# Optimization experiments

Hardware: AMD Instinct MI355X
Metric: run time of the kernel (lower is better)

## Reference

```python
import jax, jax.numpy as jnp
import numpy as np

B, R, S, C, H, MLP = 4, 32, 4, 128, 4, 512  # batch, resolution, box_size, dim, heads, mlp_dim
N = S ** 3            # tokens per window = 64
NW = (R // S) ** 3    # windows per batch element = 512
SHIFT = S // 2


def _layernorm(x, g, b):
    m = jnp.mean(x, axis=-1, keepdims=True)
    v = jnp.var(x, axis=-1, keepdims=True)
    return (x - m) * jax.lax.rsqrt(v + 1e-5) * g + b


def _box_partition(x):
    # x: (b, R, R, R, C) -> (b*NW, N, C)
    b = x.shape[0]
    x = x.reshape(b, R // S, S, R // S, S, R // S, S, C)
    x = x.transpose(0, 1, 3, 5, 2, 4, 6, 7)
    return x.reshape(-1, N, C)


def _box_reverse(w, b):
    # w: (b*NW, N, C) -> (b, R, R, R, C)
    x = w.reshape(b, R // S, R // S, R // S, S, S, S, C)
    x = x.transpose(0, 1, 4, 2, 5, 3, 6, 7)
    return x.reshape(b, R, R, R, C)


def setup_inputs():
    key = jax.random.key(0)
    ks = jax.random.split(key, 8)
    f = lambda k, sh: jax.random.normal(k, sh, dtype=jnp.float32) * 0.02
    x = jax.random.normal(ks[0], (B, R ** 3, C), dtype=jnp.float32)
    qkv_w = f(ks[1], (3 * C, C))
    rpb_table = f(ks[2], ((3 * S - 1) ** 3, H))
    proj_w = f(ks[3], (C, C))
    proj_b = jnp.zeros((C,), jnp.float32)
    norm1_g = jnp.ones((C,), jnp.float32)
    norm1_b = jnp.zeros((C,), jnp.float32)
    norm2_g = jnp.ones((C,), jnp.float32)
    norm2_b = jnp.zeros((C,), jnp.float32)
    mlp_w1 = f(ks[4], (MLP, C))
    mlp_b1 = jnp.zeros((MLP,), jnp.float32)
    mlp_w2 = f(ks[5], (C, MLP))
    mlp_b2 = jnp.zeros((C,), jnp.float32)
    # relative position index (N, N), int constant
    coords = np.stack(np.meshgrid(*([np.arange(S)] * 3), indexing='ij')).reshape(3, -1)
    rel = coords[:, :, None] - coords[:, None, :]
    rel = rel.transpose(1, 2, 0) + (S - 1)
    rel[..., 0] *= (2 * S - 1) ** 2
    rel[..., 1] *= (2 * S - 1)
    rel_index = jnp.asarray(rel.sum(-1), jnp.int32)
    # shifted-window additive attention mask (NW, N, N)
    img = np.zeros((1, R, R, R, 1), np.float32)
    sl = (slice(0, -S), slice(-S, -SHIFT), slice(-SHIFT, None))
    cnt = 0
    for a in sl:
        for b2 in sl:
            for c in sl:
                img[:, a, b2, c, :] = cnt
                cnt += 1
    m = img.reshape(1, R // S, S, R // S, S, R // S, S, 1)
    m = m.transpose(0, 1, 3, 5, 2, 4, 6, 7).reshape(-1, N)
    am = m[:, None, :] - m[:, :, None]
    attn_mask = jnp.asarray(np.where(am != 0, -100.0, 0.0).astype(np.float32))
    return dict(x=x, qkv_w=qkv_w, rpb_table=rpb_table, proj_w=proj_w, proj_b=proj_b,
                norm1_g=norm1_g, norm1_b=norm1_b, norm2_g=norm2_g, norm2_b=norm2_b,
                mlp_w1=mlp_w1, mlp_b1=mlp_b1, mlp_w2=mlp_w2, mlp_b2=mlp_b2,
                attn_mask=attn_mask, rel_index=rel_index)


def reference(x, qkv_w, rpb_table, proj_w, proj_b, norm1_g, norm1_b,
              norm2_g, norm2_b, mlp_w1, mlp_b1, mlp_w2, mlp_b2,
              attn_mask, rel_index):
    scale = (C // H) ** -0.5
    shortcut = x
    xn = _layernorm(x, norm1_g, norm1_b).reshape(B, R, R, R, C)
    xs = jnp.roll(xn, (-SHIFT,) * 3, axis=(1, 2, 3))
    w = _box_partition(xs)  # (B*NW, N, C)
    qkv = (w @ qkv_w.T).reshape(-1, N, 3, H, C // H).transpose(2, 0, 3, 1, 4)
    q, k, v = qkv[0] * scale, qkv[1], qkv[2]  # (B*NW, H, N, hd)
    attn = jnp.einsum('whnd,whmd->whnm', q, k)
    bias = rpb_table[rel_index].transpose(2, 0, 1)  # (H, N, N)
    attn = attn + bias[None]
    attn = attn.reshape(B, NW, H, N, N) + attn_mask[None, :, None]
    attn = jax.nn.softmax(attn.reshape(-1, H, N, N), axis=-1)
    out = jnp.einsum('whnm,whmd->whnd', attn, v).transpose(0, 2, 1, 3).reshape(-1, N, C)
    out = out @ proj_w.T + proj_b
    xm = _box_reverse(out, B)
    xm = jnp.roll(xm, (SHIFT,) * 3, axis=(1, 2, 3)).reshape(B, -1, C)
    x1 = shortcut + 0.5 * xm
    h = _layernorm(x1, norm2_g, norm2_b)
    h = jax.nn.gelu(h @ mlp_w1.T + mlp_b1, approximate=False) @ mlp_w2.T + mlp_b2
    return x1 + 0.5 * h
```

## Files before the change

kernel.cpp:

```cpp
#include <hip/hip_runtime.h>
#include <hip/hip_bf16.h>

typedef unsigned short u16;
typedef unsigned int u32;
typedef short bf16x8 __attribute__((ext_vector_type(8)));
typedef float f32x4 __attribute__((ext_vector_type(4)));

__device__ __forceinline__ u16 f2bf(float f) {
  union { float f; u32 i; } v; v.f = f;
  u32 x = v.i;
  x += 0x7fff + ((x >> 16) & 1);
  return (u16)(x >> 16);
}
__device__ __forceinline__ u32 pack2(float a, float b) {
  return (u32)f2bf(a) | ((u32)f2bf(b) << 16);
}
__device__ __forceinline__ u32 cvtpk2(float a, float b) {
  __hip_bfloat162 t = __float22bfloat162_rn(float2{a, b});
  union { __hip_bfloat162 h; u32 u; } v; v.h = t; return v.u;
}
__device__ __forceinline__ float fastrcp(float x) {
  float r;
  asm("v_rcp_f32 %0, %1" : "=v"(r) : "v"(x));
  return r;
}

#define L2E 1.4426950408889634f


__global__ void prep_kernel(const float* __restrict__ rpb, const int* __restrict__ rel,
                            const float* __restrict__ qkv_w, const float* __restrict__ proj_w,
                            const float* __restrict__ w1, const float* __restrict__ w2,
                            float* __restrict__ bias_t, u16* __restrict__ qkv_f,
                            u16* __restrict__ proj_f, u16* __restrict__ w1f,
                            u16* __restrict__ w2f) {
  const int bid = blockIdx.x;
  if (bid < 64) {
    const int idx = bid * 256 + threadIdx.x;
    const int h = idx >> 12, rm = idx & 4095;
    const int r = rm >> 6, c = rm & 63;
    bias_t[h * 4096 + c * 64 + r] = rpb[rel[rm] * 4 + h] * L2E;
    return;
  }
  const int i4 = (bid - 64) * 256 + threadIdx.x;
  const int e = i4 * 4;
  const float scale = 0.17677669529663687f * L2E;
  float4 v; u16* dst;
  if (e < 49152) {
    v = *(const float4*)(qkv_w + e);
    if (e < 16384) { v.x *= scale; v.y *= scale; v.z *= scale; v.w *= scale; }
    const int row = e >> 7, col = e & 127;
    const int tile = (row >> 4) * 4 + (col >> 5);
    const int lane = ((col >> 3) & 3) * 16 + (row & 15);
    dst = qkv_f + tile * 512 + lane * 8 + (col & 7);
  } else if (e < 65536) {
    const int le = e - 49152;
    v = *(const float4*)(proj_w + le);
    const int row = le >> 7, col = le & 127;
    const int tile = (row >> 4) * 4 + (col >> 5);
    const int lane = ((col >> 3) & 3) * 16 + (row & 15);
    dst = proj_f + tile * 512 + lane * 8 + (col & 7);
  } else if (e < 131072) {
    const int le = e - 65536;
    v = *(const float4*)(w1 + le);
    const int row = le >> 7, col = le & 127;
    const int tile = (row >> 4) * 4 + (col >> 5);
    const int lane = ((col >> 3) & 3) * 16 + (row & 15);
    dst = w1f + tile * 512 + lane * 8 + (col & 7);
  } else {
    const int le = e - 131072;
    v = *(const float4*)(w2 + le);
    const int row = le >> 9, col = le & 511;
    const int tile = (row >> 4) * 16 + (col >> 5);
    const int lane = ((col >> 3) & 3) * 16 + (row & 15);
    dst = w2f + tile * 512 + lane * 8 + (col & 7);
  }
  *(uint2*)dst = make_uint2(pack2(v.x, v.y), pack2(v.z, v.w));
}

__global__ __launch_bounds__(512, 4) void fused_kernel(
    const float* __restrict__ x, const u16* __restrict__ qkv_f,
    const u16* __restrict__ proj_f, const float* __restrict__ proj_b,
    const float* __restrict__ n1g, const float* __restrict__ n1b,
    const float* __restrict__ amask, const float* __restrict__ bias_t,
    const u16* __restrict__ w1f, const float* __restrict__ b1,
    const u16* __restrict__ w2f, const float* __restrict__ b2,
    const float* __restrict__ n2g, const float* __restrict__ n2b,
    float* __restrict__ out)
{
  __shared__ __align__(16) unsigned char lds[70656];
  __shared__ int srcIdx[64];
  u16* xw = (u16*)(lds);
  u16* qb = (u16*)(lds + 17408);
  u16* kb = (u16*)(lds + 34816);
  u16* vt = (u16*)(lds + 52224);
  unsigned char* Pb = lds;
  u16* Ob = kb;
  float* x1f = (float*)(lds);
  u16* xn  = (u16*)(lds + 34816);
  u16* h1c0 = (u16*)(lds + 52224);
  u16* h1c1 = (u16*)(lds + 61440);

  const int tid = threadIdx.x;
  const int wv = tid >> 6, lane = tid & 63;
  const int l15 = lane & 15, lg = lane >> 4;
  const int hw = wv & 3;
  const int half = wv >> 2;

  const int wIdx = blockIdx.x;
  const int bb = wIdx >> 9, ww = wIdx & 511;
  const int w0 = ww >> 6, w1i = (ww >> 3) & 7, w2i = ww & 7;
  const bool hasMask = (w0 == 7) || (w1i == 7) || (w2i == 7);

  {
    const int tok = tid >> 3;
    const int qt = tid & 7;
    const int s0 = tok >> 4, s1 = (tok >> 2) & 3, s2 = tok & 3;
    const int p0 = (w0 * 4 + s0 + 2) & 31;
    const int p1 = (w1i * 4 + s1 + 2) & 31;
    const int p2 = (w2i * 4 + s2 + 2) & 31;
    const int src = (bb << 15) + (p0 << 10) + (p1 << 5) + p2;
    if (qt == 0) srcIdx[tok] = src;
    float v[16]; float s = 0.f, sq = 0.f;
    const float4* p4 = (const float4*)(x + src * 128 + qt * 16);
    #pragma unroll
    for (int i = 0; i < 4; ++i) {
      float4 u = p4[i];
      v[i * 4 + 0] = u.x; v[i * 4 + 1] = u.y; v[i * 4 + 2] = u.z; v[i * 4 + 3] = u.w;
      s += u.x + u.y + u.z + u.w;
      sq += u.x * u.x + u.y * u.y + u.z * u.z + u.w * u.w;
    }
    s  += __shfl_xor(s, 1);  s  += __shfl_xor(s, 2);  s  += __shfl_xor(s, 4);
    sq += __shfl_xor(sq, 1); sq += __shfl_xor(sq, 2); sq += __shfl_xor(sq, 4);
    const float mean = s * 0.0078125f;
    const float var  = sq * 0.0078125f - mean * mean;
    const float rstd = rsqrtf(var + 1e-5f);
    u16* dst = xw + tok * 136 + qt * 16;
    #pragma unroll
    for (int i = 0; i < 16; i += 2) {
      const int c = qt * 16 + i;
      float y0 = (v[i]     - mean) * rstd * n1g[c]     + n1b[c];
      float y1 = (v[i + 1] - mean) * rstd * n1g[c + 1] + n1b[c + 1];
      *(u32*)(dst + i) = cvtpk2(y0, y1);
    }
  }
  __syncthreads();

  const f32x4 zero4 = {0.f, 0.f, 0.f, 0.f};

  bf16x8 xa[2][4];
  #pragma unroll
  for (int ti = 0; ti < 2; ++ti)
    #pragma unroll
    for (int ks = 0; ks < 4; ++ks)
      xa[ti][ks] = *(const bf16x8*)(xw + ((half * 2 + ti) * 16 + l15) * 136 + ks * 32 + lg * 8);

  #pragma unroll
  for (int cc = 0; cc < 4; ++cc) {
    const u16* wp = qkv_f + (cc * 4 + hw) * 4 * 512 + lane * 8;
    f32x4 acc[2] = {zero4, zero4};
    #pragma unroll
    for (int ks = 0; ks < 4; ++ks) {
      const bf16x8 bfr = *(const bf16x8*)(wp + ks * 512);
      acc[0] = __builtin_amdgcn_mfma_f32_16x16x32_bf16(bfr, xa[0][ks], acc[0], 0, 0, 0);
      acc[1] = __builtin_amdgcn_mfma_f32_16x16x32_bf16(bfr, xa[1][ks], acc[1], 0, 0, 0);
    }
    u16* dstbuf = (cc < 2) ? qb : kb;
    const int ob = (cc & 1) * 64 + hw * 16 + lg * 4;
    #pragma unroll
    for (int ti = 0; ti < 2; ++ti) {
      const int token = (half * 2 + ti) * 16 + l15;
      uint2 pk = make_uint2(cvtpk2(acc[ti][0], acc[ti][1]), cvtpk2(acc[ti][2], acc[ti][3]));
      *(uint2*)(dstbuf + token * 136 + ob) = pk;
    }
  }
  #pragma unroll
  for (int cc = 4; cc < 6; ++cc) {
    const u16* wp = qkv_f + (cc * 4 + hw) * 4 * 512 + lane * 8;
    f32x4 acc[2] = {zero4, zero4};
    #pragma unroll
    for (int ks = 0; ks < 4; ++ks) {
      const bf16x8 bfr = *(const bf16x8*)(wp + ks * 512);
      acc[0] = __builtin_amdgcn_mfma_f32_16x16x32_bf16(xa[0][ks], bfr, acc[0], 0, 0, 0);
      acc[1] = __builtin_amdgcn_mfma_f32_16x16x32_bf16(xa[1][ks], bfr, acc[1], 0, 0, 0);
    }
    const int cvch = (cc - 4) * 64 + hw * 16 + l15;
    #pragma unroll
    for (int ti = 0; ti < 2; ++ti) {
      uint2 pk = make_uint2(cvtpk2(acc[ti][0], acc[ti][1]), cvtpk2(acc[ti][2], acc[ti][3]));
      *(uint2*)(vt + cvch * 72 + (half * 2 + ti) * 16 + lg * 4) = pk;
    }
  }
  __syncthreads();

  f32x4 s[2][4];
  {
    bf16x8 qa[2];
    #pragma unroll
    for (int ti = 0; ti < 2; ++ti)
      qa[ti] = *(const bf16x8*)(qb + ((half * 2 + ti) * 16 + l15) * 136 + hw * 32 + lg * 8);
    #pragma unroll
    for (int tj = 0; tj < 4; ++tj) {
      const bf16x8 kf = *(const bf16x8*)(kb + (tj * 16 + l15) * 136 + hw * 32 + lg * 8);
      s[0][tj] = __builtin_amdgcn_mfma_f32_16x16x32_bf16(qa[0], kf, zero4, 0, 0, 0);
      s[1][tj] = __builtin_amdgcn_mfma_f32_16x16x32_bf16(qa[1], kf, zero4, 0, 0, 0);
    }
  }
  #pragma unroll
  for (int ti = 0; ti < 2; ++ti) {
    const int rowb = (half * 2 + ti) * 16 + lg * 4;
    #pragma unroll
    for (int tj = 0; tj < 4; ++tj) {
      const int col = tj * 16 + l15;
      const float4 bt = *(const float4*)(bias_t + hw * 4096 + col * 64 + rowb);
      s[ti][tj][0] += bt.x; s[ti][tj][1] += bt.y;
      s[ti][tj][2] += bt.z; s[ti][tj][3] += bt.w;
    }
  }
  if (hasMask) {
    #pragma unroll
    for (int ti = 0; ti < 2; ++ti) {
      #pragma unroll
      for (int r = 0; r < 4; ++r) {
        const int row = (half * 2 + ti) * 16 + lg * 4 + r;
        const float* mp = amask + ww * 4096 + row * 64;
        #pragma unroll
        for (int tj = 0; tj < 4; ++tj)
          s[ti][tj][r] = fmaf(mp[tj * 16 + l15], L2E, s[ti][tj][r]);
      }
    }
  }
  __syncthreads();

  unsigned char* ps = Pb + wv * 4096;
  #pragma unroll
  for (int ti = 0; ti < 2; ++ti) {
    #pragma unroll
    for (int r = 0; r < 4; ++r) {
      float e[4]; float sum = 0.f;
      #pragma unroll
      for (int tj = 0; tj < 4; ++tj) {
        e[tj] = exp2f(s[ti][tj][r]);
        sum += e[tj];
      }
      sum += __shfl_xor(sum, 1);
      sum += __shfl_xor(sum, 2);
      sum += __shfl_xor(sum, 4);
      sum += __shfl_xor(sum, 8);
      const float rcp = fastrcp(sum);
      const int row = ti * 16 + lg * 4 + r;
      const int swz = (row & 7) << 4;
      #pragma unroll
      for (int tj = 0; tj < 4; ++tj) {
        const int byteoff = (row * 128 + (tj * 16 + l15) * 2) ^ swz;
        *(u16*)(ps + byteoff) = f2bf(e[tj] * rcp);
      }
    }
  }

  {
    f32x4 oacc[2][2] = {{zero4, zero4}, {zero4, zero4}};
    #pragma unroll
    for (int ks = 0; ks < 2; ++ks) {
      bf16x8 pa[2], vb[2];
      #pragma unroll
      for (int ti = 0; ti < 2; ++ti) {
        const int row = ti * 16 + l15;
        const int slot = ((ks * 4 + lg) ^ (row & 7)) << 4;
        pa[ti] = *(const bf16x8*)(ps + row * 128 + slot);
      }
      #pragma unroll
      for (int tj = 0; tj < 2; ++tj)
        vb[tj] = *(const bf16x8*)(vt + (hw * 32 + tj * 16 + l15) * 72 + ks * 32 + lg * 8);
      #pragma unroll
      for (int ti = 0; ti < 2; ++ti)
        #pragma unroll
        for (int tj = 0; tj < 2; ++tj)
          oacc[ti][tj] = __builtin_amdgcn_mfma_f32_16x16x32_bf16(vb[tj], pa[ti], oacc[ti][tj], 0, 0, 0);
    }
    #pragma unroll
    for (int ti = 0; ti < 2; ++ti)
      #pragma unroll
      for (int tj = 0; tj < 2; ++tj) {
        const int token = (half * 2 + ti) * 16 + l15;
        uint2 pk = make_uint2(cvtpk2(oacc[ti][tj][0], oacc[ti][tj][1]),
                              cvtpk2(oacc[ti][tj][2], oacc[ti][tj][3]));
        *(uint2*)(Ob + token * 136 + hw * 32 + tj * 16 + lg * 4) = pk;
      }
  }
  __syncthreads();

  bf16x8 oafr[2][4];
  #pragma unroll
  for (int ti = 0; ti < 2; ++ti)
    #pragma unroll
    for (int ks = 0; ks < 4; ++ks)
      oafr[ti][ks] = *(const bf16x8*)(Ob + ((half * 2 + ti) * 16 + l15) * 136 + ks * 32 + lg * 8);
  #pragma unroll
  for (int cc = 0; cc < 2; ++cc) {
    const u16* wp = proj_f + (cc * 4 + hw) * 4 * 512 + lane * 8;
    f32x4 acc[2] = {zero4, zero4};
    #pragma unroll
    for (int ks = 0; ks < 4; ++ks) {
      const bf16x8 bfr = *(const bf16x8*)(wp + ks * 512);
      acc[0] = __builtin_amdgcn_mfma_f32_16x16x32_bf16(bfr, oafr[0][ks], acc[0], 0, 0, 0);
      acc[1] = __builtin_amdgcn_mfma_f32_16x16x32_bf16(bfr, oafr[1][ks], acc[1], 0, 0, 0);
    }
    const int cb = cc * 64 + hw * 16 + lg * 4;
    const float4 pb4 = *(const float4*)(proj_b + cb);
    #pragma unroll
    for (int ti = 0; ti < 2; ++ti) {
      const int token = (half * 2 + ti) * 16 + l15;
      const int src = srcIdx[token];
      float4 xr = *(const float4*)(x + src * 128 + cb);
      xr.x += 0.5f * (acc[ti][0] + pb4.x);
      xr.y += 0.5f * (acc[ti][1] + pb4.y);
      xr.z += 0.5f * (acc[ti][2] + pb4.z);
      xr.w += 0.5f * (acc[ti][3] + pb4.w);
      *(float4*)(x1f + token * 132 + cb) = xr;
    }
  }
  __syncthreads();

  {
    const int tok = tid >> 3;
    const int qt = tid & 7;
    float v[16]; float s2 = 0.f, sq = 0.f;
    const float4* p4 = (const float4*)(x1f + tok * 132 + qt * 16);
    #pragma unroll
    for (int i = 0; i < 4; ++i) {
      float4 u = p4[i];
      v[i * 4 + 0] = u.x; v[i * 4 + 1] = u.y; v[i * 4 + 2] = u.z; v[i * 4 + 3] = u.w;
      s2 += u.x + u.y + u.z + u.w;
      sq += u.x * u.x + u.y * u.y + u.z * u.z + u.w * u.w;
    }
    s2 += __shfl_xor(s2, 1); s2 += __shfl_xor(s2, 2); s2 += __shfl_xor(s2, 4);
    sq += __shfl_xor(sq, 1); sq += __shfl_xor(sq, 2); sq += __shfl_xor(sq, 4);
    const float mean = s2 * 0.0078125f;
    const float var  = sq * 0.0078125f - mean * mean;
    const float rstd = rsqrtf(var + 1e-5f);
    u16* dst = xn + tok * 136 + qt * 16;
    #pragma unroll
    for (int i = 0; i < 16; i += 2) {
      const int c = qt * 16 + i;
      float y0 = (v[i]     - mean) * rstd * n2g[c]     + n2b[c];
      float y1 = (v[i + 1] - mean) * rstd * n2g[c + 1] + n2b[c + 1];
      *(u32*)(dst + i) = cvtpk2(y0, y1);
    }
  }
  __syncthreads();

  f32x4 acc2[2][2] = {{zero4, zero4}, {zero4, zero4}};
  #pragma unroll 1
  for (int oc = 0; oc < 8; ++oc) {
    u16* h1c = (oc & 1) ? h1c1 : h1c0;
    f32x4 a1[2] = {zero4, zero4};
    const u16* wp1 = w1f + (oc * 4 + hw) * 4 * 512 + lane * 8;
    #pragma unroll
    for (int ks = 0; ks < 4; ++ks) {
      const bf16x8 bfr = *(const bf16x8*)(wp1 + ks * 512);
      #pragma unroll
      for (int ti = 0; ti < 2; ++ti) {
        const bf16x8 afr = *(const bf16x8*)(xn + ((half * 2 + ti) * 16 + l15) * 136 + ks * 32 + lg * 8);
        a1[ti] = __builtin_amdgcn_mfma_f32_16x16x32_bf16(bfr, afr, a1[ti], 0, 0, 0);
      }
    }
    bf16x8 w2r[2][2];
    #pragma unroll
    for (int tj = 0; tj < 2; ++tj)
      #pragma unroll
      for (int ks = 0; ks < 2; ++ks)
        w2r[tj][ks] = *(const bf16x8*)(w2f + (((hw * 2 + tj) * 16) + (oc * 2 + ks)) * 512 + lane * 8);

    const int olb = hw * 16 + lg * 4;
    const float4 b14 = *(const float4*)(b1 + oc * 64 + olb);
    const float b1v[4] = {b14.x, b14.y, b14.z, b14.w};
    #pragma unroll
    for (int ti = 0; ti < 2; ++ti) {
      float g[4];
      #pragma unroll
      for (int r = 0; r < 4; ++r) {
        const float u = a1[ti][r] + b1v[r];
        const float t = u + 0.044715f * u * u * u;
        g[r] = u * fastrcp(1.0f + exp2f(-2.302207725f * t));
      }
      const int token = (half * 2 + ti) * 16 + l15;
      *(uint2*)(h1c + token * 72 + olb) = make_uint2(cvtpk2(g[0], g[1]), cvtpk2(g[2], g[3]));
    }
    __syncthreads();

    #pragma unroll
    for (int ks = 0; ks < 2; ++ks) {
      bf16x8 afr[2];
      #pragma unroll
      for (int ti = 0; ti < 2; ++ti)
        afr[ti] = *(const bf16x8*)(h1c + ((half * 2 + ti) * 16 + l15) * 72 + ks * 32 + lg * 8);
      #pragma unroll
      for (int ti = 0; ti < 2; ++ti)
        #pragma unroll
        for (int tj = 0; tj < 2; ++tj)
          acc2[ti][tj] = __builtin_amdgcn_mfma_f32_16x16x32_bf16(w2r[tj][ks], afr[ti], acc2[ti][tj], 0, 0, 0);
    }
  }

  #pragma unroll
  for (int tj = 0; tj < 2; ++tj) {
    const int cb = hw * 32 + tj * 16 + lg * 4;
    const float4 b24 = *(const float4*)(b2 + cb);
    #pragma unroll
    for (int ti = 0; ti < 2; ++ti) {
      const int token = (half * 2 + ti) * 16 + l15;
      const int src = srcIdx[token];
      float4 xr = *(const float4*)(x1f + token * 132 + cb);
      xr.x += 0.5f * (acc2[ti][tj][0] + b24.x);
      xr.y += 0.5f * (acc2[ti][tj][1] + b24.y);
      xr.z += 0.5f * (acc2[ti][tj][2] + b24.z);
      xr.w += 0.5f * (acc2[ti][tj][3] + b24.w);
      *(float4*)(out + src * 128 + cb) = xr;
    }
  }
}

extern "C" void kernel_launch(void* const* d_in, const int* in_sizes, int n_in,
                              void* d_out, int out_size, void* d_ws, size_t ws_size,
                              hipStream_t stream) {
  const float* x      = (const float*)d_in[0];
  const float* qkv_w  = (const float*)d_in[1];
  const float* rpb    = (const float*)d_in[2];
  const float* proj_w = (const float*)d_in[3];
  const float* proj_b = (const float*)d_in[4];
  const float* n1g    = (const float*)d_in[5];
  const float* n1b    = (const float*)d_in[6];
  const float* n2g    = (const float*)d_in[7];
  const float* n2b    = (const float*)d_in[8];
  const float* w1     = (const float*)d_in[9];
  const float* b1     = (const float*)d_in[10];
  const float* w2     = (const float*)d_in[11];
  const float* b2     = (const float*)d_in[12];
  const float* amask  = (const float*)d_in[13];
  const int*   rel    = (const int*)d_in[14];
  float* out  = (float*)d_out;

  unsigned char* ws = (unsigned char*)d_ws;
  float* bias_t = (float*)(ws);
  u16* qkv_f  = (u16*)(ws + 65536);
  u16* proj_f = (u16*)(ws + 163840);
  u16* w1f    = (u16*)(ws + 196608);
  u16* w2f    = (u16*)(ws + 327680);

  prep_kernel<<<256, 256, 0, stream>>>(rpb, rel, qkv_w, proj_w, w1, w2,
                                       bias_t, qkv_f, proj_f, w1f, w2f);
  fused_kernel<<<2048, 512, 0, stream>>>(x, qkv_f, proj_f, proj_b, n1g, n1b, amask, bias_t,
                                         w1f, b1, w2f, b2, n2g, n2b, out);
}
```

Baseline: 144.1 us.

## Shrink LDS footprint via buffer aliasing and bf16 residual to raise occupancy

```diff
diff --git a/kernel.cpp b/kernel.cpp
--- a/kernel.cpp
+++ b/kernel.cpp
@@ -18,6 +18,12 @@
 __device__ __forceinline__ u32 cvtpk2(float a, float b) {
   __hip_bfloat162 t = __float22bfloat162_rn(float2{a, b});
   union { __hip_bfloat162 h; u32 u; } v; v.h = t; return v.u;
+}
+__device__ __forceinline__ u16 f2bf1(float a) {
+  return (u16)cvtpk2(a, a);
+}
+__device__ __forceinline__ float bf2f(u16 u) {
+  union { u32 i; float f; } v; v.i = ((u32)u) << 16; return v.f;
 }
 __device__ __forceinline__ float fastrcp(float x) {
   float r;
@@ -78,7 +84,7 @@
   *(uint2*)dst = make_uint2(pack2(v.x, v.y), pack2(v.z, v.w));
 }
 
-__global__ __launch_bounds__(512, 4) void fused_kernel(
+__global__ __launch_bounds__(512, 6) void fused_kernel(
     const float* __restrict__ x, const u16* __restrict__ qkv_f,
     const u16* __restrict__ proj_f, const float* __restrict__ proj_b,
     const float* __restrict__ n1g, const float* __restrict__ n1b,
@@ -88,18 +94,18 @@
     const float* __restrict__ n2g, const float* __restrict__ n2b,
     float* __restrict__ out)
 {
-  __shared__ __align__(16) unsigned char lds[70656];
+  __shared__ __align__(16) unsigned char lds[53248];
   __shared__ int srcIdx[64];
   u16* xw = (u16*)(lds);
-  u16* qb = (u16*)(lds + 17408);
-  u16* kb = (u16*)(lds + 34816);
-  u16* vt = (u16*)(lds + 52224);
+  u16* qb = (u16*)(lds);
+  u16* kb = (u16*)(lds + 17408);
+  u16* vt = (u16*)(lds + 34816);
   unsigned char* Pb = lds;
-  u16* Ob = kb;
-  float* x1f = (float*)(lds);
-  u16* xn  = (u16*)(lds + 34816);
-  u16* h1c0 = (u16*)(lds + 52224);
-  u16* h1c1 = (u16*)(lds + 61440);
+  u16* Ob = (u16*)(lds);
+  u16* x1b = (u16*)(lds + 17408);
+  u16* xn  = (u16*)(lds);
+  u16* h1c0 = (u16*)(lds + 34816);
+  u16* h1c1 = (u16*)(lds + 44032);
 
   const int tid = threadIdx.x;
   const int wv = tid >> 6, lane = tid & 63;
@@ -154,6 +160,7 @@
     #pragma unroll
     for (int ks = 0; ks < 4; ++ks)
       xa[ti][ks] = *(const bf16x8*)(xw + ((half * 2 + ti) * 16 + l15) * 136 + ks * 32 + lg * 8);
+  __syncthreads();
 
   #pragma unroll
   for (int cc = 0; cc < 4; ++cc) {
@@ -253,41 +260,40 @@
       #pragma unroll
       for (int tj = 0; tj < 4; ++tj) {
         const int byteoff = (row * 128 + (tj * 16 + l15) * 2) ^ swz;
-        *(u16*)(ps + byteoff) = f2bf(e[tj] * rcp);
-      }
-    }
-  }
-
-  {
-    f32x4 oacc[2][2] = {{zero4, zero4}, {zero4, zero4}};
-    #pragma unroll
-    for (int ks = 0; ks < 2; ++ks) {
-      bf16x8 pa[2], vb[2];
-      #pragma unroll
-      for (int ti = 0; ti < 2; ++ti) {
-        const int row = ti * 16 + l15;
-        const int slot = ((ks * 4 + lg) ^ (row & 7)) << 4;
-        pa[ti] = *(const bf16x8*)(ps + row * 128 + slot);
-      }
+        *(u16*)(ps + byteoff) = f2bf1(e[tj] * rcp);
+      }
+    }
+  }
+  f32x4 oacc[2][2] = {{zero4, zero4}, {zero4, zero4}};
+  #pragma unroll
+  for (int ks = 0; ks < 2; ++ks) {
+    bf16x8 pa[2], vb[2];
+    #pragma unroll
+    for (int ti = 0; ti < 2; ++ti) {
+      const int row = ti * 16 + l15;
+      const int slot = ((ks * 4 + lg) ^ (row & 7)) << 4;
+      pa[ti] = *(const bf16x8*)(ps + row * 128 + slot);
+    }
+    #pragma unroll
+    for (int tj = 0; tj < 2; ++tj)
+      vb[tj] = *(const bf16x8*)(vt + (hw * 32 + tj * 16 + l15) * 72 + ks * 32 + lg * 8);
+    #pragma unroll
+    for (int ti = 0; ti < 2; ++ti)
       #pragma unroll
       for (int tj = 0; tj < 2; ++tj)
-        vb[tj] = *(const bf16x8*)(vt + (hw * 32 + tj * 16 + l15) * 72 + ks * 32 + lg * 8);
-      #pragma unroll
-      for (int ti = 0; ti < 2; ++ti)
-        #pragma unroll
-        for (int tj = 0; tj < 2; ++tj)
-          oacc[ti][tj] = __builtin_amdgcn_mfma_f32_16x16x32_bf16(vb[tj], pa[ti], oacc[ti][tj], 0, 0, 0);
-    }
-    #pragma unroll
-    for (int ti = 0; ti < 2; ++ti)
-      #pragma unroll
-      for (int tj = 0; tj < 2; ++tj) {
-        const int token = (half * 2 + ti) * 16 + l15;
-        uint2 pk = make_uint2(cvtpk2(oacc[ti][tj][0], oacc[ti][tj][1]),
-                              cvtpk2(oacc[ti][tj][2], oacc[ti][tj][3]));
-        *(uint2*)(Ob + token * 136 + hw * 32 + tj * 16 + lg * 4) = pk;
-      }
-  }
+        oacc[ti][tj] = __builtin_amdgcn_mfma_f32_16x16x32_bf16(vb[tj], pa[ti], oacc[ti][tj], 0, 0, 0);
+  }
+  __syncthreads();
+
+  #pragma unroll
+  for (int ti = 0; ti < 2; ++ti)
+    #pragma unroll
+    for (int tj = 0; tj < 2; ++tj) {
+      const int token = (half * 2 + ti) * 16 + l15;
+      uint2 pk = make_uint2(cvtpk2(oacc[ti][tj][0], oacc[ti][tj][1]),
+                            cvtpk2(oacc[ti][tj][2], oacc[ti][tj][3]));
+      *(uint2*)(Ob + token * 136 + hw * 32 + tj * 16 + lg * 4) = pk;
+    }
   __syncthreads();
 
   bf16x8 oafr[2][4];
@@ -317,7 +323,7 @@
       xr.y += 0.5f * (acc[ti][1] + pb4.y);
       xr.z += 0.5f * (acc[ti][2] + pb4.z);
       xr.w += 0.5f * (acc[ti][3] + pb4.w);
-      *(float4*)(x1f + token * 132 + cb) = xr;
+      *(uint2*)(x1b + token * 136 + cb) = make_uint2(cvtpk2(xr.x, xr.y), cvtpk2(xr.z, xr.w));
     }
   }
   __syncthreads();
@@ -326,13 +332,18 @@
     const int tok = tid >> 3;
     const int qt = tid & 7;
     float v[16]; float s2 = 0.f, sq = 0.f;
-    const float4* p4 = (const float4*)(x1f + tok * 132 + qt * 16);
-    #pragma unroll
-    for (int i = 0; i < 4; ++i) {
-      float4 u = p4[i];
-      v[i * 4 + 0] = u.x; v[i * 4 + 1] = u.y; v[i * 4 + 2] = u.z; v[i * 4 + 3] = u.w;
-      s2 += u.x + u.y + u.z + u.w;
-      sq += u.x * u.x + u.y * u.y + u.z * u.z + u.w * u.w;
+    const uint4* p4 = (const uint4*)(x1b + tok * 136 + qt * 16);
+    #pragma unroll
+    for (int i = 0; i < 2; ++i) {
+      uint4 u = p4[i];
+      u32 w4[4] = {u.x, u.y, u.z, u.w};
+      #pragma unroll
+      for (int j = 0; j < 4; ++j) {
+        float lo = bf2f((u16)(w4[j] & 0xffffu));
+        float hi = bf2f((u16)(w4[j] >> 16));
+        v[i * 8 + j * 2] = lo; v[i * 8 + j * 2 + 1] = hi;
+        s2 += lo + hi; sq += lo * lo + hi * hi;
+      }
     }
     s2 += __shfl_xor(s2, 1); s2 += __shfl_xor(s2, 2); s2 += __shfl_xor(s2, 4);
     sq += __shfl_xor(sq, 1); sq += __shfl_xor(sq, 2); sq += __shfl_xor(sq, 4);
@@ -411,11 +422,12 @@
     for (int ti = 0; ti < 2; ++ti) {
       const int token = (half * 2 + ti) * 16 + l15;
       const int src = srcIdx[token];
-      float4 xr = *(const float4*)(x1f + token * 132 + cb);
-      xr.x += 0.5f * (acc2[ti][tj][0] + b24.x);
-      xr.y += 0.5f * (acc2[ti][tj][1] + b24.y);
-      xr.z += 0.5f * (acc2[ti][tj][2] + b24.z);
-      xr.w += 0.5f * (acc2[ti][tj][3] + b24.w);
+      const uint2 xp = *(const uint2*)(x1b + token * 136 + cb);
+      float4 xr;
+      xr.x = bf2f((u16)(xp.x & 0xffffu)) + 0.5f * (acc2[ti][tj][0] + b24.x);
+      xr.y = bf2f((u16)(xp.x >> 16))     + 0.5f * (acc2[ti][tj][1] + b24.y);
+      xr.z = bf2f((u16)(xp.y & 0xffffu)) + 0.5f * (acc2[ti][tj][2] + b24.z);
+      xr.w = bf2f((u16)(xp.y >> 16))     + 0.5f * (acc2[ti][tj][3] + b24.w);
       *(float4*)(out + src * 128 + cb) = xr;
     }
   }
```

Measured after the change: 148.9 us. 3.3% more time.
